# Performance work log

Measured on AMD Instinct MI355X. Metric: run time of the kernel, lower is better.

## Reference

```python
import jax, jax.numpy as jnp
import numpy as np
import math

D_K = 64
DROP_P = 0.5

def setup_inputs() -> dict:
    key = jax.random.key(0)
    kq, kk, kv, km = jax.random.split(key, 4)
    B, S, d = 32, 2048, D_K
    Q = jax.random.normal(kq, (B, S, d), dtype=jnp.float32)
    K = jax.random.normal(kk, (B, S, d), dtype=jnp.float32)
    V = jax.random.normal(kv, (B, S, d), dtype=jnp.float32)
    # Bernoulli(keep_prob) mask for training-mode dropout (p=0.5)
    dropout_mask = jax.random.bernoulli(km, 1.0 - DROP_P, (B, S, S))
    return {"Q": Q, "K": K, "V": V, "dropout_mask": dropout_mask}

def reference(Q, K, V, dropout_mask):
    # attn = softmax(Q K^T / sqrt(d_k)); dropout; y = attn V
    scale = 1.0 / math.sqrt(D_K)
    scores = jnp.einsum('bqd,bkd->bqk', Q, K) * scale   # [B,S,S]
    attn = jax.nn.softmax(scores, axis=-1)
    keep_scale = 1.0 / (1.0 - DROP_P)
    attn = jnp.where(dropout_mask, attn * keep_scale, 0.0)
    y = jnp.einsum('bqk,bkd->bqd', attn, V)             # [B,S,d]
    return (y, attn)
```

## Files before the change

kernel.cpp:

```cpp
#include <hip/hip_runtime.h>
#include <hip/hip_bf16.h>
#include <stdint.h>

#define SQ 2048
#define DK 64
#define NB 32
#define TQ 32
#define EW 2064
#define SCL 0.18033688011112042f

typedef __attribute__((ext_vector_type(8))) short short8;
typedef __attribute__((ext_vector_type(4))) float f32x4;
typedef __attribute__((ext_vector_type(4))) unsigned u32x4;
typedef __attribute__((ext_vector_type(2))) unsigned u32x2;

__device__ __forceinline__ unsigned f2bf_u(float x) {
    unsigned u = __builtin_bit_cast(unsigned, x);
    u += 0x7fffu + ((u >> 16) & 1u);
    return u >> 16;
}
__device__ __forceinline__ float bf2f(unsigned h) {
    return __builtin_bit_cast(float, h << 16);
}
__device__ __forceinline__ float bf2f_hi(unsigned u) {
    return __builtin_bit_cast(float, u & 0xffff0000u);
}
__device__ __forceinline__ unsigned cvtpk_bf16(float lo, float hi) {
    unsigned r;
    asm("v_cvt_pk_bf16_f32 %0, %1, %2" : "=v"(r) : "v"(lo), "v"(hi));
    return r;
}
__device__ __forceinline__ void split8(const float* p, short8& h, short8& l) {
    f32x4 a = *(const f32x4*)p;
    f32x4 b = *(const f32x4*)(p + 4);
    #pragma unroll
    for (int j = 0; j < 4; ++j) {
        unsigned ua = f2bf_u(a[j]);
        h[j] = (short)ua; l[j] = (short)f2bf_u(a[j] - bf2f(ua));
        unsigned ub = f2bf_u(b[j]);
        h[j + 4] = (short)ub; l[j + 4] = (short)f2bf_u(b[j] - bf2f(ub));
    }
}

__global__ __launch_bounds__(256) void prep_kernel(
    const float* __restrict__ K, const float* __restrict__ V,
    unsigned short* __restrict__ Khi, unsigned short* __restrict__ Klo,
    unsigned short* __restrict__ Vt)
{
    __shared__ float vtile[64][65];
    const int t  = threadIdx.x;
    const int b  = blockIdx.x >> 5;
    const int s0 = (blockIdx.x & 31) << 6;
    const size_t base = ((size_t)b * SQ + s0) * DK + (size_t)t * 16;

    {
        short8 h0, l0, h1, l1;
        split8(K + base,     h0, l0);
        split8(K + base + 8, h1, l1);
        *(short8*)(Khi + base)     = h0;
        *(short8*)(Khi + base + 8) = h1;
        *(short8*)(Klo + base)     = l0;
        *(short8*)(Klo + base + 8) = l1;
    }
    {
        const int sr = t >> 2, dc = (t & 3) << 4;
        #pragma unroll
        for (int u = 0; u < 16; u += 4) {
            f32x4 v = *(const f32x4*)(V + base + u);
            vtile[sr][dc + u + 0] = v[0];
            vtile[sr][dc + u + 1] = v[1];
            vtile[sr][dc + u + 2] = v[2];
            vtile[sr][dc + u + 3] = v[3];
        }
    }
    __syncthreads();
    #pragma unroll
    for (int rep = 0; rep < 16; ++rep) {
        const int idx = rep * 256 + t;
        const int d = idx >> 6, s = idx & 63;
        Vt[((size_t)b * DK + d) * SQ + s0 + s] = (unsigned short)f2bf_u(vtile[s][d]);
    }
}

__global__ __launch_bounds__(256) void mkpack_kernel(
    const unsigned* __restrict__ Mk, unsigned* __restrict__ Mkb)
{
    const size_t w = (size_t)blockIdx.x * 256 + threadIdx.x;
    const unsigned* p = Mk + w * 32;
    unsigned bits = 0;
    #pragma unroll
    for (int j = 0; j < 8; ++j) {
        const u32x4 v = *(const u32x4*)(p + j * 4);
        bits |= (v[0] ? 1u : 0u) << (j * 4 + 0);
        bits |= (v[1] ? 1u : 0u) << (j * 4 + 1);
        bits |= (v[2] ? 1u : 0u) << (j * 4 + 2);
        bits |= (v[3] ? 1u : 0u) << (j * 4 + 3);
    }
    Mkb[w] = bits;
}

__global__ __launch_bounds__(1024, 4) void sdpa_main(
    const float* __restrict__ Q, const unsigned short* __restrict__ Khi,
    const unsigned short* __restrict__ Klo, const unsigned short* __restrict__ Vt,
    const unsigned* __restrict__ Mkb, float* __restrict__ Yout, float* __restrict__ Aout)
{
    __shared__ __align__(16) unsigned short e_lds[TQ][EW];
    __shared__ float yp[2][4][16][16];
    __shared__ float rsum[16][TQ];
    __shared__ float i2s[TQ];

    const int tid  = threadIdx.x;
    const int lane = tid & 63;
    const int wv   = tid >> 6;
    const int m16  = lane & 15;
    const int kq   = lane >> 4;
    const int koff = kq * 8;

    const int bx  = blockIdx.x;
    const int xcd = bx & 7;
    const int j   = bx >> 3;
    const int b   = xcd * 4 + (j >> 6);
    const int q0  = (j & 63) * TQ;

    short8 qh0[2], ql0[2], qh1[2], ql1[2];
    {
        const float* qr0 = Q + ((size_t)b * SQ + q0 + m16) * DK;
        split8(qr0 + koff,      qh0[0], ql0[0]);
        split8(qr0 + 32 + koff, qh0[1], ql0[1]);
        const float* qr1 = qr0 + 16 * DK;
        split8(qr1 + koff,      qh1[0], ql1[0]);
        split8(qr1 + 32 + koff, qh1[1], ql1[1]);
    }

    const int ks = wv;
    const u32x4 mw0 = *(const u32x4*)(Mkb + ((size_t)b * SQ + q0 + m16) * (SQ / 32) + ks * 4);
    const u32x4 mw1 = *(const u32x4*)(Mkb + ((size_t)b * SQ + q0 + 16 + m16) * (SQ / 32) + ks * 4);

    float rs0 = 0.f, rs1 = 0.f;
    {
        const size_t krow = ((size_t)b * SQ + ks * 128 + m16) * DK;
        const unsigned short* khp = Khi + krow;
        const unsigned short* klp = Klo + krow;
        const int xw = (m16 & 7) << 3;
        #pragma unroll
        for (int t = 0; t < 8; ++t) {
            const int off = t * 16 * DK;
            const short8 kh0 = *(const short8*)(khp + off + koff);
            const short8 kh1 = *(const short8*)(khp + off + 32 + koff);
            const short8 kl0 = *(const short8*)(klp + off + koff);
            const short8 kl1 = *(const short8*)(klp + off + 32 + koff);

            {
                f32x4 a0 = {0.f, 0.f, 0.f, 0.f};
                f32x4 a1 = {0.f, 0.f, 0.f, 0.f};
                a0 = __builtin_amdgcn_mfma_f32_16x16x32_bf16(kh0, qh0[0], a0, 0, 0, 0);
                a1 = __builtin_amdgcn_mfma_f32_16x16x32_bf16(kh1, qh0[1], a1, 0, 0, 0);
                a0 = __builtin_amdgcn_mfma_f32_16x16x32_bf16(kh0, ql0[0], a0, 0, 0, 0);
                a1 = __builtin_amdgcn_mfma_f32_16x16x32_bf16(kh1, ql0[1], a1, 0, 0, 0);
                a0 = __builtin_amdgcn_mfma_f32_16x16x32_bf16(kl0, qh0[0], a0, 0, 0, 0);
                a1 = __builtin_amdgcn_mfma_f32_16x16x32_bf16(kl1, qh0[1], a1, 0, 0, 0);
                const float e0 = __builtin_amdgcn_exp2f((a0[0] + a1[0]) * SCL);
                const float e1 = __builtin_amdgcn_exp2f((a0[1] + a1[1]) * SCL);
                const float e2 = __builtin_amdgcn_exp2f((a0[2] + a1[2]) * SCL);
                const float e3 = __builtin_amdgcn_exp2f((a0[3] + a1[3]) * SCL);
                rs0 += (e0 + e1) + (e2 + e3);
                const unsigned bits = (mw0[t >> 1] >> ((t & 1) * 16 + kq * 4)) & 0xfu;
                const float m0 = (bits & 1u) ? e0 : 0.f;
                const float m1 = (bits & 2u) ? e1 : 0.f;
                const float m2 = (bits & 4u) ? e2 : 0.f;
                const float m3 = (bits & 8u) ? e3 : 0.f;
                u32x2 pk;
                pk[0] = cvtpk_bf16(m0, m1);
                pk[1] = cvtpk_bf16(m2, m3);
                *(u32x2*)&e_lds[m16][(ks * 128 + t * 16 + kq * 4) ^ xw] = pk;
            }
            {
                f32x4 a0 = {0.f, 0.f, 0.f, 0.f};
                f32x4 a1 = {0.f, 0.f, 0.f, 0.f};
                a0 = __builtin_amdgcn_mfma_f32_16x16x32_bf16(kh0, qh1[0], a0, 0, 0, 0);
                a1 = __builtin_amdgcn_mfma_f32_16x16x32_bf16(kh1, qh1[1], a1, 0, 0, 0);
                a0 = __builtin_amdgcn_mfma_f32_16x16x32_bf16(kh0, ql1[0], a0, 0, 0, 0);
                a1 = __builtin_amdgcn_mfma_f32_16x16x32_bf16(kh1, ql1[1], a1, 0, 0, 0);
                a0 = __builtin_amdgcn_mfma_f32_16x16x32_bf16(kl0, qh1[0], a0, 0, 0, 0);
                a1 = __builtin_amdgcn_mfma_f32_16x16x32_bf16(kl1, qh1[1], a1, 0, 0, 0);
                const float e0 = __builtin_amdgcn_exp2f((a0[0] + a1[0]) * SCL);
                const float e1 = __builtin_amdgcn_exp2f((a0[1] + a1[1]) * SCL);
                const float e2 = __builtin_amdgcn_exp2f((a0[2] + a1[2]) * SCL);
                const float e3 = __builtin_amdgcn_exp2f((a0[3] + a1[3]) * SCL);
                rs1 += (e0 + e1) + (e2 + e3);
                const unsigned bits = (mw1[t >> 1] >> ((t & 1) * 16 + kq * 4)) & 0xfu;
                const float m0 = (bits & 1u) ? e0 : 0.f;
                const float m1 = (bits & 2u) ? e1 : 0.f;
                const float m2 = (bits & 4u) ? e2 : 0.f;
                const float m3 = (bits & 8u) ? e3 : 0.f;
                u32x2 pk;
                pk[0] = cvtpk_bf16(m0, m1);
                pk[1] = cvtpk_bf16(m2, m3);
                *(u32x2*)&e_lds[16 + m16][(ks * 128 + t * 16 + kq * 4) ^ xw] = pk;
            }
        }
    }
    rs0 += __shfl_xor(rs0, 16);
    rs0 += __shfl_xor(rs0, 32);
    rs1 += __shfl_xor(rs1, 16);
    rs1 += __shfl_xor(rs1, 32);
    if (lane < 16) {
        rsum[wv][lane]      = rs0;
        rsum[wv][16 + lane] = rs1;
    }
    __syncthreads();
    if (tid < TQ) {
        float s = 0.f;
        #pragma unroll
        for (int w = 0; w < 16; ++w) s += rsum[w][tid];
        i2s[tid] = 2.0f / s;
    }
    __syncthreads();

    const int cr = tid >> 5;
    const int cc = (tid & 31) * 8;
    const int xc = (cr & 7) << 3;
    const float i2 = i2s[cr];
    const size_t crow = ((size_t)b * SQ + q0 + cr) * SQ + cc;

    const int qg  = wv >> 3;
    const int g   = (wv >> 1) & 3;
    const int par = wv & 1;
    const int xm  = (m16 & 7) << 3;
    const int erow = qg * 16 + m16;
    const int xe  = (erow & 7) << 3;
    const unsigned short* vrow = Vt + ((size_t)b * DK + g * 16 + m16) * SQ + par * 1024;
    f32x4 acc = {0.f, 0.f, 0.f, 0.f};

    #define CSTRIPE(s)                                                            \
    {                                                                             \
        const u32x4 ev = *(const u32x4*)&e_lds[cr][((s) * 256 + cc) ^ xc];        \
        f32x4 o0, o1;                                                             \
        o0[0] = bf2f(ev[0] & 0xffffu) * i2;  o0[1] = bf2f_hi(ev[0]) * i2;         \
        o0[2] = bf2f(ev[1] & 0xffffu) * i2;  o0[3] = bf2f_hi(ev[1]) * i2;         \
        o1[0] = bf2f(ev[2] & 0xffffu) * i2;  o1[1] = bf2f_hi(ev[2]) * i2;         \
        o1[2] = bf2f(ev[3] & 0xffffu) * i2;  o1[3] = bf2f_hi(ev[3]) * i2;         \
        __builtin_nontemporal_store(o0, (f32x4*)(Aout + crow + (s) * 256));       \
        __builtin_nontemporal_store(o1, (f32x4*)(Aout + crow + (s) * 256 + 4));   \
    }
    #define PVCHUNK4(c0)                                                          \
    {                                                                             \
        _Pragma("unroll")                                                         \
        for (int c = (c0); c < (c0) + 4; ++c) {                                   \
            const int kl = par * 1024 + c * 32;                                   \
            const short8 af = *(const short8*)&e_lds[erow][(kl + koff) ^ xe];     \
            const short8 vf = *(const short8*)(vrow + c * 32 + koff);             \
            acc = __builtin_amdgcn_mfma_f32_16x16x32_bf16(af, vf, acc, 0, 0, 0);  \
        }                                                                         \
    }

    CSTRIPE(0) PVCHUNK4(0)
    CSTRIPE(1) PVCHUNK4(4)
    CSTRIPE(2) PVCHUNK4(8)
    CSTRIPE(3) PVCHUNK4(12)
    CSTRIPE(4) PVCHUNK4(16)
    CSTRIPE(5) PVCHUNK4(20)
    CSTRIPE(6) PVCHUNK4(24)
    CSTRIPE(7) PVCHUNK4(28)

    #undef PVCHUNK4
    #undef CSTRIPE

    if (par == 1) {
        #pragma unroll
        for (int r = 0; r < 4; ++r) yp[qg][g][kq * 4 + r][m16] = acc[r];
    }
    __syncthreads();
    if (par == 0) {
        #pragma unroll
        for (int r = 0; r < 4; ++r) {
            const float yv = (acc[r] + yp[qg][g][kq * 4 + r][m16]) * i2s[qg * 16 + kq * 4 + r];
            Yout[((size_t)b * SQ + q0 + qg * 16 + kq * 4 + r) * DK + g * 16 + m16] = yv;
        }
    }
}

extern "C" void kernel_launch(void* const* d_in, const int* in_sizes, int n_in,
                              void* d_out, int out_size, void* d_ws, size_t ws_size,
                              hipStream_t stream) {
    const float*    Q  = (const float*)d_in[0];
    const float*    K  = (const float*)d_in[1];
    const float*    V  = (const float*)d_in[2];
    const unsigned* Mk = (const unsigned*)d_in[3];
    float* Yout = (float*)d_out;
    float* Aout = (float*)d_out + (size_t)NB * SQ * DK;

    const size_t NEL = (size_t)NB * SQ * DK;
    unsigned short* Khi = (unsigned short*)d_ws;
    unsigned short* Klo = Khi + NEL;
    unsigned short* Vt  = Klo + NEL;
    unsigned*       Mkb = (unsigned*)(Vt + NEL);

    prep_kernel<<<dim3(NB * (SQ / 64)), dim3(256), 0, stream>>>(K, V, Khi, Klo, Vt);
    mkpack_kernel<<<dim3((NB * SQ * (SQ / 32)) / 256), dim3(256), 0, stream>>>(Mk, Mkb);
    sdpa_main<<<dim3(NB * (SQ / TQ)), dim3(1024), 0, stream>>>(
        Q, Khi, Klo, Vt, Mkb, Yout, Aout);
}
```

Before: 470.4 us.

## Halve query tile to 16 rows with 512-thread blocks, use plain attn stores

Shrinks the per-block query tile from 32 to 16 rows and uses 8 waves instead of 16. Each wave now computes scores for 256 keys of a single 16-row query group, and the PV stage splits the 64 output columns across wave pairs. The smaller LDS footprint lets more blocks share a CU and gives finer-grained scheduling. The cost is that each K/V tile is reused across half as many queries, so K/V reads from cache double. Attention-output stores also switch from nontemporal to regular stores, which changes how the large attn write stream interacts with the cache.

```diff
diff --git a/kernel.cpp b/kernel.cpp
--- a/kernel.cpp
+++ b/kernel.cpp
@@ -5,7 +5,7 @@
 #define SQ 2048
 #define DK 64
 #define NB 32
-#define TQ 32
+#define TQ 16
 #define EW 2064
 #define SCL 0.18033688011112042f
 
@@ -99,14 +99,14 @@
     Mkb[w] = bits;
 }
 
-__global__ __launch_bounds__(1024, 4) void sdpa_main(
+__global__ __launch_bounds__(512, 4) void sdpa_main(
     const float* __restrict__ Q, const unsigned short* __restrict__ Khi,
     const unsigned short* __restrict__ Klo, const unsigned short* __restrict__ Vt,
     const unsigned* __restrict__ Mkb, float* __restrict__ Yout, float* __restrict__ Aout)
 {
     __shared__ __align__(16) unsigned short e_lds[TQ][EW];
-    __shared__ float yp[2][4][16][16];
-    __shared__ float rsum[16][TQ];
+    __shared__ float yp[4][TQ][16];
+    __shared__ float rsum[8][TQ];
     __shared__ float i2s[TQ];
 
     const int tid  = threadIdx.x;
@@ -119,100 +119,66 @@
     const int bx  = blockIdx.x;
     const int xcd = bx & 7;
     const int j   = bx >> 3;
-    const int b   = xcd * 4 + (j >> 6);
-    const int q0  = (j & 63) * TQ;
-
-    short8 qh0[2], ql0[2], qh1[2], ql1[2];
-    {
-        const float* qr0 = Q + ((size_t)b * SQ + q0 + m16) * DK;
-        split8(qr0 + koff,      qh0[0], ql0[0]);
-        split8(qr0 + 32 + koff, qh0[1], ql0[1]);
-        const float* qr1 = qr0 + 16 * DK;
-        split8(qr1 + koff,      qh1[0], ql1[0]);
-        split8(qr1 + 32 + koff, qh1[1], ql1[1]);
-    }
-
-    const int ks = wv;
-    const u32x4 mw0 = *(const u32x4*)(Mkb + ((size_t)b * SQ + q0 + m16) * (SQ / 32) + ks * 4);
-    const u32x4 mw1 = *(const u32x4*)(Mkb + ((size_t)b * SQ + q0 + 16 + m16) * (SQ / 32) + ks * 4);
-
-    float rs0 = 0.f, rs1 = 0.f;
-    {
-        const size_t krow = ((size_t)b * SQ + ks * 128 + m16) * DK;
+    const int b   = xcd * 4 + (j >> 7);
+    const int q0  = (j & 127) * TQ;
+
+    short8 qh[2], ql[2];
+    {
+        const float* qrow = Q + ((size_t)b * SQ + q0 + m16) * DK;
+        split8(qrow + koff,      qh[0], ql[0]);
+        split8(qrow + 32 + koff, qh[1], ql[1]);
+    }
+
+    const unsigned* mrow = Mkb + ((size_t)b * SQ + q0 + m16) * (SQ / 32) + wv * 8;
+    const u32x4 mA = *(const u32x4*)mrow;
+    const u32x4 mB = *(const u32x4*)(mrow + 4);
+
+    float rs = 0.f;
+    {
+        const size_t krow = ((size_t)b * SQ + wv * 256 + m16) * DK;
         const unsigned short* khp = Khi + krow;
         const unsigned short* klp = Klo + krow;
         const int xw = (m16 & 7) << 3;
         #pragma unroll
-        for (int t = 0; t < 8; ++t) {
+        for (int t = 0; t < 16; ++t) {
             const int off = t * 16 * DK;
             const short8 kh0 = *(const short8*)(khp + off + koff);
             const short8 kh1 = *(const short8*)(khp + off + 32 + koff);
             const short8 kl0 = *(const short8*)(klp + off + koff);
             const short8 kl1 = *(const short8*)(klp + off + 32 + koff);
-
-            {
-                f32x4 a0 = {0.f, 0.f, 0.f, 0.f};
-                f32x4 a1 = {0.f, 0.f, 0.f, 0.f};
-                a0 = __builtin_amdgcn_mfma_f32_16x16x32_bf16(kh0, qh0[0], a0, 0, 0, 0);
-                a1 = __builtin_amdgcn_mfma_f32_16x16x32_bf16(kh1, qh0[1], a1, 0, 0, 0);
-                a0 = __builtin_amdgcn_mfma_f32_16x16x32_bf16(kh0, ql0[0], a0, 0, 0, 0);
-                a1 = __builtin_amdgcn_mfma_f32_16x16x32_bf16(kh1, ql0[1], a1, 0, 0, 0);
-                a0 = __builtin_amdgcn_mfma_f32_16x16x32_bf16(kl0, qh0[0], a0, 0, 0, 0);
-                a1 = __builtin_amdgcn_mfma_f32_16x16x32_bf16(kl1, qh0[1], a1, 0, 0, 0);
-                const float e0 = __builtin_amdgcn_exp2f((a0[0] + a1[0]) * SCL);
-                const float e1 = __builtin_amdgcn_exp2f((a0[1] + a1[1]) * SCL);
-                const float e2 = __builtin_amdgcn_exp2f((a0[2] + a1[2]) * SCL);
-                const float e3 = __builtin_amdgcn_exp2f((a0[3] + a1[3]) * SCL);
-                rs0 += (e0 + e1) + (e2 + e3);
-                const unsigned bits = (mw0[t >> 1] >> ((t & 1) * 16 + kq * 4)) & 0xfu;
-                const float m0 = (bits & 1u) ? e0 : 0.f;
-                const float m1 = (bits & 2u) ? e1 : 0.f;
-                const float m2 = (bits & 4u) ? e2 : 0.f;
-                const float m3 = (bits & 8u) ? e3 : 0.f;
-                u32x2 pk;
-                pk[0] = cvtpk_bf16(m0, m1);
-                pk[1] = cvtpk_bf16(m2, m3);
-                *(u32x2*)&e_lds[m16][(ks * 128 + t * 16 + kq * 4) ^ xw] = pk;
-            }
-            {
-                f32x4 a0 = {0.f, 0.f, 0.f, 0.f};
-                f32x4 a1 = {0.f, 0.f, 0.f, 0.f};
-                a0 = __builtin_amdgcn_mfma_f32_16x16x32_bf16(kh0, qh1[0], a0, 0, 0, 0);
-                a1 = __builtin_amdgcn_mfma_f32_16x16x32_bf16(kh1, qh1[1], a1, 0, 0, 0);
-                a0 = __builtin_amdgcn_mfma_f32_16x16x32_bf16(kh0, ql1[0], a0, 0, 0, 0);
-                a1 = __builtin_amdgcn_mfma_f32_16x16x32_bf16(kh1, ql1[1], a1, 0, 0, 0);
-                a0 = __builtin_amdgcn_mfma_f32_16x16x32_bf16(kl0, qh1[0], a0, 0, 0, 0);
-                a1 = __builtin_amdgcn_mfma_f32_16x16x32_bf16(kl1, qh1[1], a1, 0, 0, 0);
-                const float e0 = __builtin_amdgcn_exp2f((a0[0] + a1[0]) * SCL);
-                const float e1 = __builtin_amdgcn_exp2f((a0[1] + a1[1]) * SCL);
-                const float e2 = __builtin_amdgcn_exp2f((a0[2] + a1[2]) * SCL);
-                const float e3 = __builtin_amdgcn_exp2f((a0[3] + a1[3]) * SCL);
-                rs1 += (e0 + e1) + (e2 + e3);
-                const unsigned bits = (mw1[t >> 1] >> ((t & 1) * 16 + kq * 4)) & 0xfu;
-                const float m0 = (bits & 1u) ? e0 : 0.f;
-                const float m1 = (bits & 2u) ? e1 : 0.f;
-                const float m2 = (bits & 4u) ? e2 : 0.f;
-                const float m3 = (bits & 8u) ? e3 : 0.f;
-                u32x2 pk;
-                pk[0] = cvtpk_bf16(m0, m1);
-                pk[1] = cvtpk_bf16(m2, m3);
-                *(u32x2*)&e_lds[16 + m16][(ks * 128 + t * 16 + kq * 4) ^ xw] = pk;
-            }
+            f32x4 a0 = {0.f, 0.f, 0.f, 0.f};
+            f32x4 a1 = {0.f, 0.f, 0.f, 0.f};
+            a0 = __builtin_amdgcn_mfma_f32_16x16x32_bf16(kh0, qh[0], a0, 0, 0, 0);
+            a1 = __builtin_amdgcn_mfma_f32_16x16x32_bf16(kh1, qh[1], a1, 0, 0, 0);
+            a0 = __builtin_amdgcn_mfma_f32_16x16x32_bf16(kh0, ql[0], a0, 0, 0, 0);
+            a1 = __builtin_amdgcn_mfma_f32_16x16x32_bf16(kh1, ql[1], a1, 0, 0, 0);
+            a0 = __builtin_amdgcn_mfma_f32_16x16x32_bf16(kl0, qh[0], a0, 0, 0, 0);
+            a1 = __builtin_amdgcn_mfma_f32_16x16x32_bf16(kl1, qh[1], a1, 0, 0, 0);
+            const float e0 = __builtin_amdgcn_exp2f((a0[0] + a1[0]) * SCL);
+            const float e1 = __builtin_amdgcn_exp2f((a0[1] + a1[1]) * SCL);
+            const float e2 = __builtin_amdgcn_exp2f((a0[2] + a1[2]) * SCL);
+            const float e3 = __builtin_amdgcn_exp2f((a0[3] + a1[3]) * SCL);
+            rs += (e0 + e1) + (e2 + e3);
+            const unsigned mword = (t < 8) ? mA[t >> 1] : mB[(t >> 1) - 4];
+            const unsigned bits = mword >> ((t & 1) * 16 + kq * 4);
+            const float p0 = (bits & 1u) ? e0 : 0.f;
+            const float p1 = (bits & 2u) ? e1 : 0.f;
+            const float p2 = (bits & 4u) ? e2 : 0.f;
+            const float p3 = (bits & 8u) ? e3 : 0.f;
+            u32x2 pk;
+            pk[0] = cvtpk_bf16(p0, p1);
+            pk[1] = cvtpk_bf16(p2, p3);
+            *(u32x2*)&e_lds[m16][(wv * 256 + t * 16 + kq * 4) ^ xw] = pk;
         }
     }
-    rs0 += __shfl_xor(rs0, 16);
-    rs0 += __shfl_xor(rs0, 32);
-    rs1 += __shfl_xor(rs1, 16);
-    rs1 += __shfl_xor(rs1, 32);
-    if (lane < 16) {
-        rsum[wv][lane]      = rs0;
-        rsum[wv][16 + lane] = rs1;
-    }
-    __syncthreads();
-    if (tid < TQ) {
+    rs += __shfl_xor(rs, 16);
+    rs += __shfl_xor(rs, 32);
+    if (lane < 16) rsum[wv][lane] = rs;
+    __syncthreads();
+    if (tid < 16) {
         float s = 0.f;
         #pragma unroll
-        for (int w = 0; w < 16; ++w) s += rsum[w][tid];
+        for (int w = 0; w < 8; ++w) s += rsum[w][tid];
         i2s[tid] = 2.0f / s;
     }
     __syncthreads();
@@ -223,13 +189,10 @@
     const float i2 = i2s[cr];
     const size_t crow = ((size_t)b * SQ + q0 + cr) * SQ + cc;
 
-    const int qg  = wv >> 3;
-    const int g   = (wv >> 1) & 3;
-    const int par = wv & 1;
-    const int xm  = (m16 & 7) << 3;
-    const int erow = qg * 16 + m16;
-    const int xe  = (erow & 7) << 3;
-    const unsigned short* vrow = Vt + ((size_t)b * DK + g * 16 + m16) * SQ + par * 1024;
+    const int g    = wv >> 1;
+    const int par  = wv & 1;
+    const int xm   = (m16 & 7) << 3;
+    const unsigned short* vrow = Vt + ((size_t)b * DK + g * 16 + m16) * SQ;
     f32x4 acc = {0.f, 0.f, 0.f, 0.f};
 
     #define CSTRIPE(s)                                                            \
@@ -240,16 +203,16 @@
         o0[2] = bf2f(ev[1] & 0xffffu) * i2;  o0[3] = bf2f_hi(ev[1]) * i2;         \
         o1[0] = bf2f(ev[2] & 0xffffu) * i2;  o1[1] = bf2f_hi(ev[2]) * i2;         \
         o1[2] = bf2f(ev[3] & 0xffffu) * i2;  o1[3] = bf2f_hi(ev[3]) * i2;         \
-        __builtin_nontemporal_store(o0, (f32x4*)(Aout + crow + (s) * 256));       \
-        __builtin_nontemporal_store(o1, (f32x4*)(Aout + crow + (s) * 256 + 4));   \
+        *(f32x4*)(Aout + crow + (s) * 256)     = o0;                              \
+        *(f32x4*)(Aout + crow + (s) * 256 + 4) = o1;                              \
     }
     #define PVCHUNK4(c0)                                                          \
     {                                                                             \
         _Pragma("unroll")                                                         \
         for (int c = (c0); c < (c0) + 4; ++c) {                                   \
             const int kl = par * 1024 + c * 32;                                   \
-            const short8 af = *(const short8*)&e_lds[erow][(kl + koff) ^ xe];     \
-            const short8 vf = *(const short8*)(vrow + c * 32 + koff);             \
+            const short8 af = *(const short8*)&e_lds[m16][(kl + koff) ^ xm];      \
+            const short8 vf = *(const short8*)(vrow + kl + koff);                 \
             acc = __builtin_amdgcn_mfma_f32_16x16x32_bf16(af, vf, acc, 0, 0, 0);  \
         }                                                                         \
     }
@@ -268,14 +231,14 @@
 
     if (par == 1) {
         #pragma unroll
-        for (int r = 0; r < 4; ++r) yp[qg][g][kq * 4 + r][m16] = acc[r];
+        for (int r = 0; r < 4; ++r) yp[g][kq * 4 + r][m16] = acc[r];
     }
     __syncthreads();
     if (par == 0) {
         #pragma unroll
         for (int r = 0; r < 4; ++r) {
-            const float yv = (acc[r] + yp[qg][g][kq * 4 + r][m16]) * i2s[qg * 16 + kq * 4 + r];
-            Yout[((size_t)b * SQ + q0 + qg * 16 + kq * 4 + r) * DK + g * 16 + m16] = yv;
+            const float yv = (acc[r] + yp[g][kq * 4 + r][m16]) * i2s[kq * 4 + r];
+            Yout[((size_t)b * SQ + q0 + kq * 4 + r) * DK + g * 16 + m16] = yv;
         }
     }
 }
@@ -298,6 +261,6 @@
 
     prep_kernel<<<dim3(NB * (SQ / 64)), dim3(256), 0, stream>>>(K, V, Khi, Klo, Vt);
     mkpack_kernel<<<dim3((NB * SQ * (SQ / 32)) / 256), dim3(256), 0, stream>>>(Mk, Mkb);
-    sdpa_main<<<dim3(NB * (SQ / TQ)), dim3(1024), 0, stream>>>(
+    sdpa_main<<<dim3(NB * (SQ / TQ)), dim3(512), 0, stream>>>(
         Q, Khi, Klo, Vt, Mkb, Yout, Aout);
 }
```

Measured after the change: 561.7 us. +19.4%, slower.

## Merge mask-pack into prep kernel, double-buffer K loads, reorder PV and attn stores

Applied to the files above, without the earlier changes.

Folds the mask bit-packing kernel into the prep kernel as extra blocks, removing one kernel launch and the gap between launches. In the QK^T phase, K hi/lo fragments are now software-pipelined with two register sets, so the loads for the next tile are issued before the current tile's MFMAs. The PV loop now runs each MFMA chunk before its attention-output stripe store instead of after. These changes aim to hide global-load latency and launch overhead, at the cost of higher register pressure from the extra K buffers.

```diff
diff --git a/kernel.cpp b/kernel.cpp
--- a/kernel.cpp
+++ b/kernel.cpp
@@ -44,11 +44,29 @@
 
 __global__ __launch_bounds__(256) void prep_kernel(
     const float* __restrict__ K, const float* __restrict__ V,
+    const unsigned* __restrict__ Mk,
     unsigned short* __restrict__ Khi, unsigned short* __restrict__ Klo,
-    unsigned short* __restrict__ Vt)
+    unsigned short* __restrict__ Vt, unsigned* __restrict__ Mkb)
 {
     __shared__ float vtile[64][65];
-    const int t  = threadIdx.x;
+    const int t = threadIdx.x;
+
+    if (blockIdx.x >= NB * 32) {
+        const size_t w = (size_t)(blockIdx.x - NB * 32) * 256 + t;
+        const unsigned* p = Mk + w * 32;
+        unsigned bits = 0;
+        #pragma unroll
+        for (int j = 0; j < 8; ++j) {
+            const u32x4 v = *(const u32x4*)(p + j * 4);
+            bits |= (v[0] ? 1u : 0u) << (j * 4 + 0);
+            bits |= (v[1] ? 1u : 0u) << (j * 4 + 1);
+            bits |= (v[2] ? 1u : 0u) << (j * 4 + 2);
+            bits |= (v[3] ? 1u : 0u) << (j * 4 + 3);
+        }
+        Mkb[w] = bits;
+        return;
+    }
+
     const int b  = blockIdx.x >> 5;
     const int s0 = (blockIdx.x & 31) << 6;
     const size_t base = ((size_t)b * SQ + s0) * DK + (size_t)t * 16;
@@ -80,23 +98,6 @@
         const int d = idx >> 6, s = idx & 63;
         Vt[((size_t)b * DK + d) * SQ + s0 + s] = (unsigned short)f2bf_u(vtile[s][d]);
     }
-}
-
-__global__ __launch_bounds__(256) void mkpack_kernel(
-    const unsigned* __restrict__ Mk, unsigned* __restrict__ Mkb)
-{
-    const size_t w = (size_t)blockIdx.x * 256 + threadIdx.x;
-    const unsigned* p = Mk + w * 32;
-    unsigned bits = 0;
-    #pragma unroll
-    for (int j = 0; j < 8; ++j) {
-        const u32x4 v = *(const u32x4*)(p + j * 4);
-        bits |= (v[0] ? 1u : 0u) << (j * 4 + 0);
-        bits |= (v[1] ? 1u : 0u) << (j * 4 + 1);
-        bits |= (v[2] ? 1u : 0u) << (j * 4 + 2);
-        bits |= (v[3] ? 1u : 0u) << (j * 4 + 3);
-    }
-    Mkb[w] = bits;
 }
 
 __global__ __launch_bounds__(1024, 4) void sdpa_main(
@@ -142,63 +143,90 @@
         const unsigned short* khp = Khi + krow;
         const unsigned short* klp = Klo + krow;
         const int xw = (m16 & 7) << 3;
-        #pragma unroll
-        for (int t = 0; t < 8; ++t) {
-            const int off = t * 16 * DK;
-            const short8 kh0 = *(const short8*)(khp + off + koff);
-            const short8 kh1 = *(const short8*)(khp + off + 32 + koff);
-            const short8 kl0 = *(const short8*)(klp + off + koff);
-            const short8 kl1 = *(const short8*)(klp + off + 32 + koff);
-
-            {
-                f32x4 a0 = {0.f, 0.f, 0.f, 0.f};
-                f32x4 a1 = {0.f, 0.f, 0.f, 0.f};
-                a0 = __builtin_amdgcn_mfma_f32_16x16x32_bf16(kh0, qh0[0], a0, 0, 0, 0);
-                a1 = __builtin_amdgcn_mfma_f32_16x16x32_bf16(kh1, qh0[1], a1, 0, 0, 0);
-                a0 = __builtin_amdgcn_mfma_f32_16x16x32_bf16(kh0, ql0[0], a0, 0, 0, 0);
-                a1 = __builtin_amdgcn_mfma_f32_16x16x32_bf16(kh1, ql0[1], a1, 0, 0, 0);
-                a0 = __builtin_amdgcn_mfma_f32_16x16x32_bf16(kl0, qh0[0], a0, 0, 0, 0);
-                a1 = __builtin_amdgcn_mfma_f32_16x16x32_bf16(kl1, qh0[1], a1, 0, 0, 0);
-                const float e0 = __builtin_amdgcn_exp2f((a0[0] + a1[0]) * SCL);
-                const float e1 = __builtin_amdgcn_exp2f((a0[1] + a1[1]) * SCL);
-                const float e2 = __builtin_amdgcn_exp2f((a0[2] + a1[2]) * SCL);
-                const float e3 = __builtin_amdgcn_exp2f((a0[3] + a1[3]) * SCL);
-                rs0 += (e0 + e1) + (e2 + e3);
-                const unsigned bits = (mw0[t >> 1] >> ((t & 1) * 16 + kq * 4)) & 0xfu;
-                const float m0 = (bits & 1u) ? e0 : 0.f;
-                const float m1 = (bits & 2u) ? e1 : 0.f;
-                const float m2 = (bits & 4u) ? e2 : 0.f;
-                const float m3 = (bits & 8u) ? e3 : 0.f;
-                u32x2 pk;
-                pk[0] = cvtpk_bf16(m0, m1);
-                pk[1] = cvtpk_bf16(m2, m3);
-                *(u32x2*)&e_lds[m16][(ks * 128 + t * 16 + kq * 4) ^ xw] = pk;
-            }
-            {
-                f32x4 a0 = {0.f, 0.f, 0.f, 0.f};
-                f32x4 a1 = {0.f, 0.f, 0.f, 0.f};
-                a0 = __builtin_amdgcn_mfma_f32_16x16x32_bf16(kh0, qh1[0], a0, 0, 0, 0);
-                a1 = __builtin_amdgcn_mfma_f32_16x16x32_bf16(kh1, qh1[1], a1, 0, 0, 0);
-                a0 = __builtin_amdgcn_mfma_f32_16x16x32_bf16(kh0, ql1[0], a0, 0, 0, 0);
-                a1 = __builtin_amdgcn_mfma_f32_16x16x32_bf16(kh1, ql1[1], a1, 0, 0, 0);
-                a0 = __builtin_amdgcn_mfma_f32_16x16x32_bf16(kl0, qh1[0], a0, 0, 0, 0);
-                a1 = __builtin_amdgcn_mfma_f32_16x16x32_bf16(kl1, qh1[1], a1, 0, 0, 0);
-                const float e0 = __builtin_amdgcn_exp2f((a0[0] + a1[0]) * SCL);
-                const float e1 = __builtin_amdgcn_exp2f((a0[1] + a1[1]) * SCL);
-                const float e2 = __builtin_amdgcn_exp2f((a0[2] + a1[2]) * SCL);
-                const float e3 = __builtin_amdgcn_exp2f((a0[3] + a1[3]) * SCL);
-                rs1 += (e0 + e1) + (e2 + e3);
-                const unsigned bits = (mw1[t >> 1] >> ((t & 1) * 16 + kq * 4)) & 0xfu;
-                const float m0 = (bits & 1u) ? e0 : 0.f;
-                const float m1 = (bits & 2u) ? e1 : 0.f;
-                const float m2 = (bits & 4u) ? e2 : 0.f;
-                const float m3 = (bits & 8u) ? e3 : 0.f;
-                u32x2 pk;
-                pk[0] = cvtpk_bf16(m0, m1);
-                pk[1] = cvtpk_bf16(m2, m3);
-                *(u32x2*)&e_lds[16 + m16][(ks * 128 + t * 16 + kq * 4) ^ xw] = pk;
-            }
+
+        short8 ka0, ka1, la0, la1;
+        short8 kb0, kb1, lb0, lb1;
+
+        #define KLOADA(t) {                                                \
+            const int off = (t) * 16 * DK;                                 \
+            ka0 = *(const short8*)(khp + off + koff);                      \
+            ka1 = *(const short8*)(khp + off + 32 + koff);                 \
+            la0 = *(const short8*)(klp + off + koff);                      \
+            la1 = *(const short8*)(klp + off + 32 + koff); }
+        #define KLOADB(t) {                                                \
+            const int off = (t) * 16 * DK;                                 \
+            kb0 = *(const short8*)(khp + off + koff);                      \
+            kb1 = *(const short8*)(khp + off + 32 + koff);                 \
+            lb0 = *(const short8*)(klp + off + koff);                      \
+            lb1 = *(const short8*)(klp + off + 32 + koff); }
+
+        #define AITER2(t, K0, K1, L0, L1)                                                   \
+        {                                                                                   \
+                                                                              \
+            {                                                                               \
+                f32x4 a0 = {0.f, 0.f, 0.f, 0.f};                                            \
+                f32x4 a1 = {0.f, 0.f, 0.f, 0.f};                                            \
+                a0 = __builtin_amdgcn_mfma_f32_16x16x32_bf16(K0, qh0[0], a0, 0, 0, 0);      \
+                a1 = __builtin_amdgcn_mfma_f32_16x16x32_bf16(K1, qh0[1], a1, 0, 0, 0);      \
+                a0 = __builtin_amdgcn_mfma_f32_16x16x32_bf16(K0, ql0[0], a0, 0, 0, 0);      \
+                a1 = __builtin_amdgcn_mfma_f32_16x16x32_bf16(K1, ql0[1], a1, 0, 0, 0);      \
+                a0 = __builtin_amdgcn_mfma_f32_16x16x32_bf16(L0, qh0[0], a0, 0, 0, 0);      \
+                a1 = __builtin_amdgcn_mfma_f32_16x16x32_bf16(L1, qh0[1], a1, 0, 0, 0);      \
+                const float e0 = __builtin_amdgcn_exp2f((a0[0] + a1[0]) * SCL);             \
+                const float e1 = __builtin_amdgcn_exp2f((a0[1] + a1[1]) * SCL);             \
+                const float e2 = __builtin_amdgcn_exp2f((a0[2] + a1[2]) * SCL);             \
+                const float e3 = __builtin_amdgcn_exp2f((a0[3] + a1[3]) * SCL);             \
+                rs0 += (e0 + e1) + (e2 + e3);                                               \
+                const unsigned bits = (mw0[(t) >> 1] >> (((t) & 1) * 16 + kq * 4)) & 0xfu;  \
+                const float p0 = (bits & 1u) ? e0 : 0.f;                                    \
+                const float p1 = (bits & 2u) ? e1 : 0.f;                                    \
+                const float p2 = (bits & 4u) ? e2 : 0.f;                                    \
+                const float p3 = (bits & 8u) ? e3 : 0.f;                                    \
+                u32x2 pk;                                                                   \
+                pk[0] = cvtpk_bf16(p0, p1);                                                 \
+                pk[1] = cvtpk_bf16(p2, p3);                                                 \
+                *(u32x2*)&e_lds[m16][(ks * 128 + (t) * 16 + kq * 4) ^ xw] = pk;             \
+            }                                                                               \
+                                                                              \
+            {                                                                               \
+                f32x4 a0 = {0.f, 0.f, 0.f, 0.f};                                            \
+                f32x4 a1 = {0.f, 0.f, 0.f, 0.f};                                            \
+                a0 = __builtin_amdgcn_mfma_f32_16x16x32_bf16(K0, qh1[0], a0, 0, 0, 0);      \
+                a1 = __builtin_amdgcn_mfma_f32_16x16x32_bf16(K1, qh1[1], a1, 0, 0, 0);      \
+                a0 = __builtin_amdgcn_mfma_f32_16x16x32_bf16(K0, ql1[0], a0, 0, 0, 0);      \
+                a1 = __builtin_amdgcn_mfma_f32_16x16x32_bf16(K1, ql1[1], a1, 0, 0, 0);      \
+                a0 = __builtin_amdgcn_mfma_f32_16x16x32_bf16(L0, qh1[0], a0, 0, 0, 0);      \
+                a1 = __builtin_amdgcn_mfma_f32_16x16x32_bf16(L1, qh1[1], a1, 0, 0, 0);      \
+                const float e0 = __builtin_amdgcn_exp2f((a0[0] + a1[0]) * SCL);             \
+                const float e1 = __builtin_amdgcn_exp2f((a0[1] + a1[1]) * SCL);             \
+                const float e2 = __builtin_amdgcn_exp2f((a0[2] + a1[2]) * SCL);             \
+                const float e3 = __builtin_amdgcn_exp2f((a0[3] + a1[3]) * SCL);             \
+                rs1 += (e0 + e1) + (e2 + e3);                                               \
+                const unsigned bits = (mw1[(t) >> 1] >> (((t) & 1) * 16 + kq * 4)) & 0xfu;  \
+                const float p0 = (bits & 1u) ? e0 : 0.f;                                    \
+                const float p1 = (bits & 2u) ? e1 : 0.f;                                    \
+                const float p2 = (bits & 4u) ? e2 : 0.f;                                    \
+                const float p3 = (bits & 8u) ? e3 : 0.f;                                    \
+                u32x2 pk;                                                                   \
+                pk[0] = cvtpk_bf16(p0, p1);                                                 \
+                pk[1] = cvtpk_bf16(p2, p3);                                                 \
+                *(u32x2*)&e_lds[16 + m16][(ks * 128 + (t) * 16 + kq * 4) ^ xw] = pk;        \
+            }                                                                               \
         }
+
+        KLOADA(0)
+        KLOADB(1) AITER2(0, ka0, ka1, la0, la1)
+        KLOADA(2) AITER2(1, kb0, kb1, lb0, lb1)
+        KLOADB(3) AITER2(2, ka0, ka1, la0, la1)
+        KLOADA(4) AITER2(3, kb0, kb1, lb0, lb1)
+        KLOADB(5) AITER2(4, ka0, ka1, la0, la1)
+        KLOADA(6) AITER2(5, kb0, kb1, lb0, lb1)
+        KLOADB(7) AITER2(6, ka0, ka1, la0, la1)
+                  AITER2(7, kb0, kb1, lb0, lb1)
+
+        #undef AITER2
+        #undef KLOADB
+        #undef KLOADA
     }
     rs0 += __shfl_xor(rs0, 16);
     rs0 += __shfl_xor(rs0, 32);
@@ -226,12 +254,21 @@
     const int qg  = wv >> 3;
     const int g   = (wv >> 1) & 3;
     const int par = wv & 1;
-    const int xm  = (m16 & 7) << 3;
     const int erow = qg * 16 + m16;
     const int xe  = (erow & 7) << 3;
     const unsigned short* vrow = Vt + ((size_t)b * DK + g * 16 + m16) * SQ + par * 1024;
     f32x4 acc = {0.f, 0.f, 0.f, 0.f};
 
+    #define PVCHUNK4(c0)                                                          \
+    {                                                                             \
+        _Pragma("unroll")                                                         \
+        for (int c = (c0); c < (c0) + 4; ++c) {                                   \
+            const int kl = par * 1024 + c * 32;                                   \
+            const short8 af = *(const short8*)&e_lds[erow][(kl + koff) ^ xe];     \
+            const short8 vf = *(const short8*)(vrow + c * 32 + koff);             \
+            acc = __builtin_amdgcn_mfma_f32_16x16x32_bf16(af, vf, acc, 0, 0, 0);  \
+        }                                                                         \
+    }
     #define CSTRIPE(s)                                                            \
     {                                                                             \
         const u32x4 ev = *(const u32x4*)&e_lds[cr][((s) * 256 + cc) ^ xc];        \
@@ -243,28 +280,18 @@
         __builtin_nontemporal_store(o0, (f32x4*)(Aout + crow + (s) * 256));       \
         __builtin_nontemporal_store(o1, (f32x4*)(Aout + crow + (s) * 256 + 4));   \
     }
-    #define PVCHUNK4(c0)                                                          \
-    {                                                                             \
-        _Pragma("unroll")                                                         \
-        for (int c = (c0); c < (c0) + 4; ++c) {                                   \
-            const int kl = par * 1024 + c * 32;                                   \
-            const short8 af = *(const short8*)&e_lds[erow][(kl + koff) ^ xe];     \
-            const short8 vf = *(const short8*)(vrow + c * 32 + koff);             \
-            acc = __builtin_amdgcn_mfma_f32_16x16x32_bf16(af, vf, acc, 0, 0, 0);  \
-        }                                                                         \
-    }
-
-    CSTRIPE(0) PVCHUNK4(0)
-    CSTRIPE(1) PVCHUNK4(4)
-    CSTRIPE(2) PVCHUNK4(8)
-    CSTRIPE(3) PVCHUNK4(12)
-    CSTRIPE(4) PVCHUNK4(16)
-    CSTRIPE(5) PVCHUNK4(20)
-    CSTRIPE(6) PVCHUNK4(24)
-    CSTRIPE(7) PVCHUNK4(28)
-
+
+    PVCHUNK4(0)  CSTRIPE(0)
+    PVCHUNK4(4)  CSTRIPE(1)
+    PVCHUNK4(8)  CSTRIPE(2)
+    PVCHUNK4(12) CSTRIPE(3)
+    PVCHUNK4(16) CSTRIPE(4)
+    PVCHUNK4(20) CSTRIPE(5)
+    PVCHUNK4(24) CSTRIPE(6)
+    PVCHUNK4(28) CSTRIPE(7)
+
+    #undef CSTRIPE
     #undef PVCHUNK4
-    #undef CSTRIPE
 
     if (par == 1) {
         #pragma unroll
@@ -296,8 +323,9 @@
     unsigned short* Vt  = Klo + NEL;
     unsigned*       Mkb = (unsigned*)(Vt + NEL);
 
-    prep_kernel<<<dim3(NB * (SQ / 64)), dim3(256), 0, stream>>>(K, V, Khi, Klo, Vt);
-    mkpack_kernel<<<dim3((NB * SQ * (SQ / 32)) / 256), dim3(256), 0, stream>>>(Mk, Mkb);
+    const int NPREP = NB * 32;
+    const int NMKP  = (int)((size_t)NB * SQ * (SQ / 32) / 256);
+    prep_kernel<<<dim3(NPREP + NMKP), dim3(256), 0, stream>>>(K, V, Mk, Khi, Klo, Vt, Mkb);
     sdpa_main<<<dim3(NB * (SQ / TQ)), dim3(1024), 0, stream>>>(
         Q, Khi, Klo, Vt, Mkb, Yout, Aout);
 }
```

After: 462.5 us. No clear change (-1.7%).
